# Kernel tuning notes

Measured on AMD Instinct MI355X. Metric: run time of the kernel, lower is better.

The kernel has to match this reference:

```python
import jax, jax.numpy as jnp
import numpy as np

_EPS = 1e-3            # distance_eps
_COEFF = 0.42 * 0.2 * 332.0
_LEN_NH = 1.015
_CUT_E = -0.5
_CUT_D = 3.6
_CUT_GAP = 3


def collect_neighbors(x, edge_idx):
    # x: (B, N, D), edge_idx: (B, N, K) -> (B, N, K, D)
    return jax.vmap(lambda xb, eb: xb[eb])(x, edge_idx)


def normed_vec(v):
    return v / jnp.sqrt(jnp.sum(v * v, axis=-1, keepdims=True) + _EPS)


def setup_inputs() -> dict:
    key = jax.random.key(0)
    k1, k2, k3 = jax.random.split(key, 3)
    B, N, K = 4, 16384, 64
    X = jax.random.normal(k1, (B, N, 4, 3), dtype=jnp.float32) * 3.0
    C = jnp.sort(jax.random.randint(k2, (B, N), 1, 9), axis=-1).astype(jnp.int64)
    edge_idx = jax.random.randint(k3, (B, N, K), 0, N).astype(jnp.int64)
    mask_ij = jnp.ones((B, N, K), dtype=jnp.float32)
    return {"X": X, "C": C, "edge_idx": edge_idx, "mask_ij": mask_ij}


def reference(X, C, edge_idx, mask_ij):
    B, N = X.shape[0], X.shape[1]
    # gather neighbor backbone atoms: (B, N, K, 4, 3)
    X_j = collect_neighbors(X.reshape(B, N, 12), edge_idx).reshape(B, N, -1, 4, 3)

    # previous residue (replicate-pad at front)
    X_prev = jnp.concatenate([X[:, :1], X[:, :-1]], axis=1)
    C_prev_i = X_prev[:, :, 2, :]          # carbonyl C of residue i-1
    N_i = X[:, :, 0, :]
    Ca_i = X[:, :, 1, :]

    # virtual hydrogen placement
    u_NH = normed_vec(normed_vec(N_i - C_prev_i) + normed_vec(N_i - Ca_i))
    H_i = N_i + _LEN_NH * u_NH             # (B, N, 3)

    Nq = N_i[:, :, None, :]                # (B, N, 1, 3)
    Hq = H_i[:, :, None, :]
    O_j = X_j[:, :, :, 3, :]               # (B, N, K, 3)
    C_j = X_j[:, :, :, 2, :]

    invD = lambda a, b: 1.0 / jnp.sqrt(jnp.sum((a - b) ** 2, axis=-1) + _EPS)
    U_ij = _COEFF * (invD(Nq, O_j) - invD(Nq, C_j) + invD(Hq, C_j) - invD(Hq, O_j))

    D_NO = jnp.sqrt(jnp.sum((Nq - O_j) ** 2, axis=-1) + _EPS)
    mask_cut_D = (D_NO < _CUT_D).astype(jnp.float32)

    # locality mask: same chain and |i-j| < cutoff_gap (note jx == edge_idx)
    Cn = collect_neighbors(C[..., None], edge_idx)[..., 0]          # (B, N, K)
    dij = jnp.abs(edge_idx - jnp.arange(N)[None, :, None])
    mask_local = ((dij < _CUT_GAP) & (C[:, :, None] == Cn)).astype(jnp.float32)
    mask_nonlocal = 1.0 - mask_local

    # NOTE: in the source, F.pad(C,[1,0])[:,1:] reproduces C itself, so
    # mask_i reduces to (C > 0); we replicate that math faithfully.
    C_prev = jnp.concatenate([jnp.zeros_like(C[:, :1]), C], axis=1)[:, 1:]
    mask_i = ((C > 0) & (C == C_prev)).astype(jnp.float32)
    mask_internal = mask_i[..., None] * (Cn > 0).astype(jnp.float32)

    mask_hb_ij = mask_ij * mask_nonlocal * mask_cut_D * mask_internal
    hbonds = mask_hb_ij * (U_ij < _CUT_E).astype(jnp.float32)
    return hbonds, mask_hb_ij, H_i[:, :, None, :]
```

## Files before the change

### kernel.cpp

```cpp
#include <hip/hip_runtime.h>

static __device__ __forceinline__ float sq3(float x, float y, float z) {
    return __fadd_rn(__fadd_rn(__fmul_rn(x, x), __fmul_rn(y, y)), __fmul_rn(z, z));
}

__global__ __launch_bounds__(256) void setup_kernel(
    const float* __restrict__ X,
    const int*   __restrict__ C,
    float*  __restrict__ outH,
    float4* __restrict__ T,
    int N, int rows)
{
    const float EPS   = 0.001f;
    const float LENNH = 1.015f;

    int row = blockIdx.x * blockDim.x + threadIdx.x;
    if (row >= rows) return;
    int i = row & (N - 1);

    const float* xi = X + (size_t)row * 12;
    float4 a4  = *(const float4*)xi;
    float2 a2  = *(const float2*)(xi + 4);
    float2 c01 = *(const float2*)(xi + 6);
    float4 co  = *(const float4*)(xi + 8);
    float nx = a4.x, ny = a4.y, nz = a4.z;
    float cax = a4.w, cay = a2.x, caz = a2.y;

    if (T) {
        T[2 * (size_t)row]     = make_float4(c01.x, c01.y, co.x, co.y);
        T[2 * (size_t)row + 1] = make_float4(co.z, co.w, __int_as_float(C[row]), 0.0f);
    }

    int prow = (i == 0) ? row : row - 1;
    const float* xp = X + (size_t)prow * 12;
    float2 p2 = *(const float2*)(xp + 6);
    float px = p2.x, py = p2.y, pz = xp[8];

    float ax = __fsub_rn(nx, px), ay = __fsub_rn(ny, py), az = __fsub_rn(nz, pz);
    float s1 = __fsqrt_rn(__fadd_rn(sq3(ax, ay, az), EPS));
    ax = __fdiv_rn(ax, s1); ay = __fdiv_rn(ay, s1); az = __fdiv_rn(az, s1);
    float bx = __fsub_rn(nx, cax), by = __fsub_rn(ny, cay), bz = __fsub_rn(nz, caz);
    float s2 = __fsqrt_rn(__fadd_rn(sq3(bx, by, bz), EPS));
    bx = __fdiv_rn(bx, s2); by = __fdiv_rn(by, s2); bz = __fdiv_rn(bz, s2);
    float ux = __fadd_rn(ax, bx), uy = __fadd_rn(ay, by), uz = __fadd_rn(az, bz);
    float s3 = __fsqrt_rn(__fadd_rn(sq3(ux, uy, uz), EPS));
    ux = __fdiv_rn(ux, s3); uy = __fdiv_rn(uy, s3); uz = __fdiv_rn(uz, s3);

    float* ho = outH + (size_t)row * 3;
    ho[0] = __fadd_rn(nx, __fmul_rn(LENNH, ux));
    ho[1] = __fadd_rn(ny, __fmul_rn(LENNH, uy));
    ho[2] = __fadd_rn(nz, __fmul_rn(LENNH, uz));
}

static __device__ __forceinline__ void edge_math(
    float nx, float ny, float nz, float hx, float hy, float hz,
    int Ci, int i, int j, float mij, float4 t0, float4 t1,
    float& hb, float& mhb)
{
    const float EPS   = 0.001f;
    const float COEFF = (float)(0.42 * 0.2 * 332.0);

    float cjx = t0.x, cjy = t0.y, cjz = t0.z;
    float ojx = t0.w, ojy = t1.x, ojz = t1.y;
    int   Cn  = __float_as_int(t1.z);

    float dx = __fsub_rn(nx, ojx), dy = __fsub_rn(ny, ojy), dz = __fsub_rn(nz, ojz);
    float dno = __fsqrt_rn(__fadd_rn(sq3(dx, dy, dz), EPS));
    float iNO = __fdiv_rn(1.0f, dno);
    dx = __fsub_rn(nx, cjx); dy = __fsub_rn(ny, cjy); dz = __fsub_rn(nz, cjz);
    float iNC = __fdiv_rn(1.0f, __fsqrt_rn(__fadd_rn(sq3(dx, dy, dz), EPS)));
    dx = __fsub_rn(hx, cjx); dy = __fsub_rn(hy, cjy); dz = __fsub_rn(hz, cjz);
    float iHC = __fdiv_rn(1.0f, __fsqrt_rn(__fadd_rn(sq3(dx, dy, dz), EPS)));
    dx = __fsub_rn(hx, ojx); dy = __fsub_rn(hy, ojy); dz = __fsub_rn(hz, ojz);
    float iHO = __fdiv_rn(1.0f, __fsqrt_rn(__fadd_rn(sq3(dx, dy, dz), EPS)));

    float U = __fmul_rn(COEFF, __fsub_rn(__fadd_rn(__fsub_rn(iNO, iNC), iHC), iHO));

    int dij = j - i; if (dij < 0) dij = -dij;
    float m_local    = ((dij < 3) && (Ci == Cn)) ? 1.0f : 0.0f;
    float m_nonlocal = __fsub_rn(1.0f, m_local);
    float m_cutD     = (dno < 3.6f) ? 1.0f : 0.0f;
    float m_i        = (Ci > 0) ? 1.0f : 0.0f;
    float m_int      = __fmul_rn(m_i, (Cn > 0) ? 1.0f : 0.0f);

    mhb = __fmul_rn(__fmul_rn(__fmul_rn(mij, m_nonlocal), m_cutD), m_int);
    hb  = __fmul_rn(mhb, (U < -0.5f) ? 1.0f : 0.0f);
}

static __device__ __forceinline__ float4 shflxor4(float4 v, int m) {
    float4 r;
    r.x = __shfl_xor(v.x, m, 64);
    r.y = __shfl_xor(v.y, m, 64);
    r.z = __shfl_xor(v.z, m, 64);
    r.w = __shfl_xor(v.w, m, 64);
    return r;
}

__global__ __launch_bounds__(256) void edge_kernel_pair2(
    const int*   __restrict__ C,
    const int*   __restrict__ E,
    const float* __restrict__ M,
    const float* __restrict__ H,
    const float* __restrict__ X,
    const float4* __restrict__ T,
    float* __restrict__ outHB,
    float* __restrict__ outMK,
    int N, int rows)
{
    int gtid = blockIdx.x * blockDim.x + threadIdx.x;
    int row  = gtid >> 6;
    if (row >= rows) return;
    int lane = threadIdx.x & 63;
    int i = row & (N - 1);
    int b = row >> 14;

    int urow = __builtin_amdgcn_readfirstlane(row);
    const float* xi = X + (size_t)urow * 12;
    float nx = xi[0], ny = xi[1], nz = xi[2];
    const float* hi = H + (size_t)urow * 3;
    float hx = hi[0], hy = hi[1], hz = hi[2];
    int Ci = C[urow];

    size_t base = (size_t)row * 64;
    int   jall = E[base + lane];
    float mall = M[base + lane];

    int e    = lane >> 1;
    int half = lane & 1;

    int jA = __shfl(jall, e, 64);
    int jB = __shfl(jall, 32 + e, 64);

    const float4* Tb = T + ((size_t)b << 15);
    float4 vA = Tb[2 * (size_t)jA + half];
    float4 vB = Tb[2 * (size_t)jB + (half ^ 1)];

    float4 vAx = shflxor4(vA, 1);
    float4 vBx = shflxor4(vB, 1);

    int   eMine = half ? (32 + e) : e;
    int   jMine = half ? jB : jA;
    float mMine = __shfl(mall, eMine, 64);
    float4 t0 = half ? vB : vA;
    float4 t1 = half ? vBx : vAx;

    float hb, mk;
    edge_math(nx, ny, nz, hx, hy, hz, Ci, i, jMine, mMine, t0, t1, hb, mk);

    int src = (lane < 32) ? (lane << 1) : (((lane & 31) << 1) | 1);
    float hbO = __shfl(hb, src, 64);
    float mkO = __shfl(mk, src, 64);

    outHB[base + lane] = hbO;
    outMK[base + lane] = mkO;
}

__global__ __launch_bounds__(256) void edge_kernel_noT(
    const float* __restrict__ X,
    const int*   __restrict__ C,
    const int*   __restrict__ E,
    const float* __restrict__ M,
    const float* __restrict__ H,
    float* __restrict__ outHB,
    float* __restrict__ outMK,
    int N, int rows)
{
    int tid = blockIdx.x * blockDim.x + threadIdx.x;
    int row = tid >> 6;
    if (row >= rows) return;
    int k = tid & 63;
    int i = row & (N - 1);
    int b = row >> 14;

    int urow = __builtin_amdgcn_readfirstlane(row);
    const float* xi = X + (size_t)urow * 12;
    float nx = xi[0], ny = xi[1], nz = xi[2];
    const float* hi = H + (size_t)urow * 3;
    float hx = hi[0], hy = hi[1], hz = hi[2];
    int Ci = C[urow];

    size_t eoff = (size_t)row * 64 + (size_t)k;
    int j = E[eoff];
    float mij = M[eoff];

    const float* xj = X + ((size_t)b * (size_t)N + (size_t)j) * 12;
    float2 cj01 = *(const float2*)(xj + 6);
    float4 v4   = *(const float4*)(xj + 8);
    int Cn = C[(size_t)b * (size_t)N + (size_t)j];

    float4 t0 = make_float4(cj01.x, cj01.y, v4.x, v4.y);
    float4 t1 = make_float4(v4.z, v4.w, __int_as_float(Cn), 0.0f);
    float hb, mhb;
    edge_math(nx, ny, nz, hx, hy, hz, Ci, i, j, mij, t0, t1, hb, mhb);

    outHB[eoff] = hb;
    outMK[eoff] = mhb;
}

extern "C" void kernel_launch(void* const* d_in, const int* in_sizes, int n_in,
                              void* d_out, int out_size, void* d_ws, size_t ws_size,
                              hipStream_t stream) {
    const float* X = (const float*)d_in[0];
    const int*   C = (const int*)d_in[1];
    const int*   E = (const int*)d_in[2];
    const float* M = (const float*)d_in[3];

    int rows = in_sizes[1];
    int BNK  = in_sizes[2];
    const int N = 16384;

    float* out   = (float*)d_out;
    float* outHB = out;
    float* outMK = out + (size_t)BNK;
    float* outH  = out + 2 * (size_t)BNK;

    size_t tbytes = (size_t)rows * 32;
    bool useT = (ws_size >= tbytes) && (d_ws != nullptr);
    float4* T = useT ? (float4*)d_ws : nullptr;

    {
        int block = 256;
        int grid  = (rows + block - 1) / block;
        hipLaunchKernelGGL(setup_kernel, dim3(grid), dim3(block), 0, stream,
                           X, C, outH, T, N, rows);
    }
    if (useT) {
        int total = rows * 64;
        int block = 256;
        int grid  = (total + block - 1) / block;
        hipLaunchKernelGGL(edge_kernel_pair2, dim3(grid), dim3(block), 0, stream,
                           C, E, M, outH, X, T, outHB, outMK, N, rows);
    } else {
        int total = rows * 64;
        int block = 256;
        int grid  = (total + block - 1) / block;
        hipLaunchKernelGGL(edge_kernel_noT, dim3(grid), dim3(block), 0, stream,
                           X, C, E, M, outH, outHB, outMK, N, rows);
    }
}
```

Baseline: 34.57 us.

## Swizzle block-to-row mapping across batches and load edges directly per lane

The edge kernel now maps blocks with a swizzle that interleaves batches, so consecutive blocks (likely landing on different XCDs) work on different batch slices of the T table. This aims to improve cache locality per XCD. It also drops the shuffle-based broadcast of edge indices and the output permutation: each lane loads its two indices and its mask value directly and writes its results to the permuted positions. The cost is extra redundant index loads and strided, non-contiguous stores within a wave.

```diff
diff --git a/kernel.cpp b/kernel.cpp
--- a/kernel.cpp
+++ b/kernel.cpp
@@ -87,16 +87,16 @@
     hb  = __fmul_rn(mhb, (U < -0.5f) ? 1.0f : 0.0f);
 }
 
-static __device__ __forceinline__ float4 shflxor4(float4 v, int m) {
+static __device__ __forceinline__ float4 swapx1(float4 v) {
     float4 r;
-    r.x = __shfl_xor(v.x, m, 64);
-    r.y = __shfl_xor(v.y, m, 64);
-    r.z = __shfl_xor(v.z, m, 64);
-    r.w = __shfl_xor(v.w, m, 64);
+    r.x = __shfl_xor(v.x, 1, 64);
+    r.y = __shfl_xor(v.y, 1, 64);
+    r.z = __shfl_xor(v.z, 1, 64);
+    r.w = __shfl_xor(v.w, 1, 64);
     return r;
 }
 
-__global__ __launch_bounds__(256) void edge_kernel_pair2(
+__global__ __launch_bounds__(256) void edge_kernel_swz(
     const int*   __restrict__ C,
     const int*   __restrict__ E,
     const float* __restrict__ M,
@@ -105,14 +105,24 @@
     const float4* __restrict__ T,
     float* __restrict__ outHB,
     float* __restrict__ outMK,
-    int N, int rows)
-{
-    int gtid = blockIdx.x * blockDim.x + threadIdx.x;
-    int row  = gtid >> 6;
+    int N, int rows, int swz)
+{
+    int g = blockIdx.x;
+    int row0;
+    if (swz) {
+        int b = (g & 7) >> 1;
+        int o = ((g >> 3) << 1) | (g & 1);
+        row0 = b * N + (o << 2);
+    } else {
+        row0 = g << 2;
+    }
+    int row = row0 + (int)(threadIdx.x >> 6);
     if (row >= rows) return;
     int lane = threadIdx.x & 63;
+    int e    = lane >> 1;
+    int half = lane & 1;
+    int eM   = (half << 5) | e;
     int i = row & (N - 1);
-    int b = row >> 14;
 
     int urow = __builtin_amdgcn_readfirstlane(row);
     const float* xi = X + (size_t)urow * 12;
@@ -121,38 +131,28 @@
     float hx = hi[0], hy = hi[1], hz = hi[2];
     int Ci = C[urow];
 
-    size_t base = (size_t)row * 64;
-    int   jall = E[base + lane];
-    float mall = M[base + lane];
-
-    int e    = lane >> 1;
-    int half = lane & 1;
-
-    int jA = __shfl(jall, e, 64);
-    int jB = __shfl(jall, 32 + e, 64);
-
-    const float4* Tb = T + ((size_t)b << 15);
+    size_t base = (size_t)row << 6;
+
+    int   jA = E[base + e];
+    int   jB = E[base + 32 + e];
+    float mM = M[base + eM];
+
+    const float4* Tb = T + ((size_t)(row >> 14) << 15);
     float4 vA = Tb[2 * (size_t)jA + half];
     float4 vB = Tb[2 * (size_t)jB + (half ^ 1)];
 
-    float4 vAx = shflxor4(vA, 1);
-    float4 vBx = shflxor4(vB, 1);
-
-    int   eMine = half ? (32 + e) : e;
-    int   jMine = half ? jB : jA;
-    float mMine = __shfl(mall, eMine, 64);
+    float4 wA = swapx1(vA);
+    float4 wB = swapx1(vB);
+
     float4 t0 = half ? vB : vA;
-    float4 t1 = half ? vBx : vAx;
+    float4 t1 = half ? wB : wA;
+    int jMine = half ? jB : jA;
 
     float hb, mk;
-    edge_math(nx, ny, nz, hx, hy, hz, Ci, i, jMine, mMine, t0, t1, hb, mk);
-
-    int src = (lane < 32) ? (lane << 1) : (((lane & 31) << 1) | 1);
-    float hbO = __shfl(hb, src, 64);
-    float mkO = __shfl(mk, src, 64);
-
-    outHB[base + lane] = hbO;
-    outMK[base + lane] = mkO;
+    edge_math(nx, ny, nz, hx, hy, hz, Ci, i, jMine, mM, t0, t1, hb, mk);
+
+    outHB[base + eM] = hb;
+    outMK[base + eM] = mk;
 }
 
 __global__ __launch_bounds__(256) void edge_kernel_noT(
@@ -208,6 +208,7 @@
     int rows = in_sizes[1];
     int BNK  = in_sizes[2];
     const int N = 16384;
+    int B = rows / N;
 
     float* out   = (float*)d_out;
     float* outHB = out;
@@ -225,11 +226,10 @@
                            X, C, outH, T, N, rows);
     }
     if (useT) {
-        int total = rows * 64;
-        int block = 256;
-        int grid  = (total + block - 1) / block;
-        hipLaunchKernelGGL(edge_kernel_pair2, dim3(grid), dim3(block), 0, stream,
-                           C, E, M, outH, X, T, outHB, outMK, N, rows);
+        int grid = (rows + 3) / 4;
+        int swz  = (B == 4 && (grid % 8 == 0)) ? 1 : 0;
+        hipLaunchKernelGGL(edge_kernel_swz, dim3(grid), dim3(256), 0, stream,
+                           C, E, M, outH, X, T, outHB, outMK, N, rows, swz);
     } else {
         int total = rows * 64;
         int block = 256;
```

Measured after the change: 34.64 us. No clear change (+0.2%).
